# Kernel optimization log

Hardware: AMD Instinct MI355X
Metric: run time of the kernel (lower is better)

Reference implementation:

```python
import jax, jax.numpy as jnp
import numpy as np

B, S, D = 2, 2048, 2048
NH, NG = 16, 4          # q heads, groups
KVH = NH // NG          # kv heads = 4
HD = D // NH            # head dim = 128
ROPE_THETA = 10000.0


def _rope(t, cos, sin):
    """Rotate pairs along last dim. t: [B,S,D]; cos/sin: [S, D//2]."""
    tr = t.reshape(t.shape[:-1] + (-1, 2))  # [B,S,D/2,2] complex pairs (llama layout)
    xr, xi = tr[..., 0], tr[..., 1]
    c = cos[None, :, :]
    s = sin[None, :, :]
    yr = xr * c - xi * s
    yi = xr * s + xi * c
    return jnp.stack([yr, yi], axis=-1).reshape(t.shape)


def setup_inputs() -> dict:
    key = jax.random.key(0)
    k0, k1, k2, k3, k4 = jax.random.split(key, 5)
    scale = 1.0 / np.sqrt(D)
    x = jax.random.normal(k0, (B, S, D), jnp.float32)
    Wq = jax.random.normal(k1, (D, D), jnp.float32) * scale          # torch Linear: (out,in)
    Wk = jax.random.normal(k2, (D // NG, D), jnp.float32) * scale
    Wv = jax.random.normal(k3, (D // NG, D), jnp.float32) * scale
    Wo = jax.random.normal(k4, (D, D), jnp.float32) * scale
    mask = jnp.triu(jnp.ones((S, S), bool), k=1)[None, None]          # causal: True = masked
    return {"x": x, "Wq": Wq, "Wk": Wk, "Wv": Wv, "Wo": Wo, "mask": mask}


def reference(x, Wq, Wk, Wv, Wo, mask):
    b, s, d = x.shape
    q = x @ Wq.T                                  # [B,S,D]
    k = x @ Wk.T                                  # [B,S,D/NG]
    v = x @ Wv.T
    # repeat_kv: [B,S,KVH,HD] -> repeat each kv head NG times -> [B,S,NH,HD]
    k = jnp.repeat(k.reshape(b, s, KVH, HD), NG, axis=2).reshape(b, s, d)
    v = jnp.repeat(v.reshape(b, s, KVH, HD), NG, axis=2).reshape(b, s, d)
    # RoPE with freqs precomputed over the FULL hidden dim (as in source)
    freqs = 1.0 / (ROPE_THETA ** (jnp.arange(0, d, 2, dtype=jnp.float32) / d))  # [D/2]
    ang = jnp.arange(s, dtype=jnp.float32)[:, None] * freqs[None, :]            # [S,D/2]
    cos, sin = jnp.cos(ang), jnp.sin(ang)
    q = _rope(q, cos, sin)
    k = _rope(k, cos, sin)
    # split heads: [B,NH,S,HD]
    qh = q.reshape(b, s, NH, HD).transpose(0, 2, 1, 3)
    kh = k.reshape(b, s, NH, HD).transpose(0, 2, 1, 3)
    vh = v.reshape(b, s, NH, HD).transpose(0, 2, 1, 3)
    # NOTE: source scales by sqrt(hidden_dim), not sqrt(head_dim)
    scores = jnp.einsum('bhqd,bhkd->bhqk', qh, kh) / jnp.sqrt(jnp.float32(d))
    scores = jnp.where(mask, -jnp.inf, scores)
    probs = jax.nn.softmax(scores, axis=-1)
    out = jnp.einsum('bhqk,bhkd->bhqd', probs, vh)
    out = out.transpose(0, 2, 1, 3).reshape(b, s, d)
    return out @ Wo.T  # dropout is identity in eval
```

## Files before the change

### kernel.cpp

```cpp
#include <hip/hip_runtime.h>
#include <hip/hip_bf16.h>
#include <stdint.h>

typedef unsigned short u16;
typedef u16 u16x4 __attribute__((ext_vector_type(4)));
typedef unsigned u32x4 __attribute__((ext_vector_type(4)));
typedef __bf16 bf16x8 __attribute__((ext_vector_type(8)));
typedef float f32x4 __attribute__((ext_vector_type(4)));
typedef float f32x16 __attribute__((ext_vector_type(16)));

#define DEVI __device__ __forceinline__

DEVI u16 f2b(float f) {
  __hip_bfloat16 h = __float2bfloat16(f);
  return __builtin_bit_cast(u16, h);
}

DEVI unsigned pk2(float lo, float hi) {
  return (unsigned)f2b(lo) | ((unsigned)f2b(hi) << 16);
}

DEVI f32x4 mfma16(bf16x8 a, bf16x8 b, f32x4 c) {
  return __builtin_amdgcn_mfma_f32_16x16x32_bf16(a, b, c, 0, 0, 0);
}

DEVI f32x16 mfma32(bf16x8 a, bf16x8 b, f32x16 c) {
  return __builtin_amdgcn_mfma_f32_32x32x16_bf16(a, b, c, 0, 0, 0);
}

DEVI void gld_lds16(const u16* g, u16* l) {
  __builtin_amdgcn_global_load_lds(
      (const __attribute__((address_space(1))) unsigned int*)g,
      (__attribute__((address_space(3))) unsigned int*)l, 16, 0, 0);
}

__global__ void cvt_all(const float4* __restrict__ x, const float4* __restrict__ wq,
                        const float4* __restrict__ wk, const float4* __restrict__ wv,
                        const float4* __restrict__ wo,
                        u16x4* __restrict__ xb, u16x4* __restrict__ wqb,
                        u16x4* __restrict__ wkb, u16x4* __restrict__ wvb,
                        u16x4* __restrict__ wob) {
  long i = (long)blockIdx.x * 256 + threadIdx.x;
  const float4* src; u16x4* dst; long o;
  if (i < 2097152)      { src = x;  dst = xb;  o = i; }
  else if (i < 3145728) { src = wq; dst = wqb; o = i - 2097152; }
  else if (i < 3407872) { src = wk; dst = wkb; o = i - 3145728; }
  else if (i < 3670016) { src = wv; dst = wvb; o = i - 3407872; }
  else                  { src = wo; dst = wob; o = i - 3670016; }
  float4 v = src[o];
  u16x4 r = { f2b(v.x), f2b(v.y), f2b(v.z), f2b(v.w) };
  dst[o] = r;
}

__global__ void rope_table(float* __restrict__ cosT, float* __restrict__ sinT) {
  int i = blockIdx.x * 256 + threadIdx.x;
  int s = i >> 10, p = i & 1023;
  float freq = exp2f((float)p * -0.012976281620653759f);
  float ang = (float)s * freq;
  float sv, cv;
  __sincosf(ang, &sv, &cv);
  cosT[i] = cv;
  sinT[i] = sv;
}

__global__ __launch_bounds__(256)
void gemm_qkv(const u16* __restrict__ A, const u16* __restrict__ wq,
              const u16* __restrict__ wk, const u16* __restrict__ wv,
              float* __restrict__ Qtmp, float* __restrict__ Ktmp,
              u16* __restrict__ Vtp) {
  __shared__ __align__(16) u16 lds[2][2][4096];
  const int tid = threadIdx.x;
  const int lane = tid & 63;
  const int w = tid >> 6;
  const int wr = w >> 1, wc = w & 1;
  const int bx = blockIdx.x;
  const int m0 = blockIdx.y << 7, n0 = bx << 7;
  const int K = 2048;

  const u16* Bw;
  int mode;
  if (bx < 16)      { Bw = wq + (size_t)n0 * K;          mode = 0; }
  else if (bx < 20) { Bw = wk + (size_t)(n0 - 2048) * K; mode = 1; }
  else              { Bw = wv + (size_t)(n0 - 2560) * K; mode = 2; }

  const int srow = tid >> 2;
  const int schunk = (tid & 3) << 3;
  const u16* ga0 = A + (size_t)(m0 + srow) * K + schunk;
  const u16* gb0 = Bw + (size_t)srow * K + schunk;
  const size_t rstep = (size_t)64 * K;

  f32x4 acc[4][4] = {};
  const int nk = K >> 5;
  int cur = 0;

  {
    u16* la = &lds[0][0][tid << 3];
    u16* lb = &lds[0][1][tid << 3];
    gld_lds16(ga0, la);
    gld_lds16(ga0 + rstep, la + 2048);
    gld_lds16(gb0, lb);
    gld_lds16(gb0 + rstep, lb + 2048);
  }
  __syncthreads();

  const int l15 = lane & 15;
  const int kcol = (lane >> 4) << 3;
  const int arow = ((wr << 6) + l15) << 5;
  const int brow = ((wc << 6) + l15) << 5;

  for (int kt = 0; kt < nk; ++kt) {
    if (kt + 1 < nk) {
      const u16* ga = ga0 + ((size_t)(kt + 1) << 5);
      const u16* gb = gb0 + ((size_t)(kt + 1) << 5);
      u16* la = &lds[cur ^ 1][0][tid << 3];
      u16* lb = &lds[cur ^ 1][1][tid << 3];
      gld_lds16(ga, la);
      gld_lds16(ga + rstep, la + 2048);
      gld_lds16(gb, lb);
      gld_lds16(gb + rstep, lb + 2048);
    }
    const u16* la = &lds[cur][0][0];
    const u16* lb = &lds[cur][1][0];
    bf16x8 af[4], bfr[4];
#pragma unroll
    for (int mi = 0; mi < 4; ++mi)
      af[mi] = *(const bf16x8*)&la[arow + (mi << 9) + kcol];
#pragma unroll
    for (int ni = 0; ni < 4; ++ni)
      bfr[ni] = *(const bf16x8*)&lb[brow + (ni << 9) + kcol];
#pragma unroll
    for (int mi = 0; mi < 4; ++mi)
#pragma unroll
      for (int ni = 0; ni < 4; ++ni)
        acc[mi][ni] = mfma16(af[mi], bfr[ni], acc[mi][ni]);
    __syncthreads();
    cur ^= 1;
  }

  const int crow = (lane >> 4) << 2;
  const int ccol = lane & 15;
  if (mode == 0) {
#pragma unroll
    for (int mi = 0; mi < 4; ++mi) {
      int row = m0 + (wr << 6) + (mi << 4) + crow;
#pragma unroll
      for (int ni = 0; ni < 4; ++ni) {
        int col = n0 + (wc << 6) + (ni << 4) + ccol;
#pragma unroll
        for (int rr = 0; rr < 4; ++rr)
          Qtmp[(size_t)(row + rr) * 2048 + col] = acc[mi][ni][rr];
      }
    }
  } else if (mode == 1) {
#pragma unroll
    for (int mi = 0; mi < 4; ++mi) {
      int row = m0 + (wr << 6) + (mi << 4) + crow;
#pragma unroll
      for (int ni = 0; ni < 4; ++ni) {
        int col = (n0 - 2048) + (wc << 6) + (ni << 4) + ccol;
#pragma unroll
        for (int rr = 0; rr < 4; ++rr)
          Ktmp[(size_t)(row + rr) * 512 + col] = acc[mi][ni][rr];
      }
    }
  } else {
#pragma unroll
    for (int mi = 0; mi < 4; ++mi) {
      int sg = m0 + (wr << 6) + (mi << 4) + crow;
      int b = sg >> 11, s = sg & 2047;
#pragma unroll
      for (int ni = 0; ni < 4; ++ni) {
        int n = (n0 - 2560) + (wc << 6) + (ni << 4) + ccol;
        u16x4 pk = { f2b(acc[mi][ni][0]), f2b(acc[mi][ni][1]),
                     f2b(acc[mi][ni][2]), f2b(acc[mi][ni][3]) };
        *(u16x4*)&Vtp[((size_t)((b << 2) + (n >> 7)) * 128 + (n & 127)) * 2048 + s] = pk;
      }
    }
  }
}

__global__ __launch_bounds__(256)
void gemm_bt(const u16* __restrict__ A, const u16* __restrict__ Bw,
             float* __restrict__ C, int M, int N, int K) {
  __shared__ __align__(16) u16 lds[2][2][4096];
  const int tid = threadIdx.x;
  const int lane = tid & 63;
  const int w = tid >> 6;
  const int wr = w >> 1, wc = w & 1;
  const int m0 = blockIdx.y << 7, n0 = blockIdx.x << 7;

  const int srow = tid >> 2;
  const int schunk = (tid & 3) << 3;
  const u16* ga0 = A + (size_t)(m0 + srow) * K + schunk;
  const u16* gb0 = Bw + (size_t)(n0 + srow) * K + schunk;
  const size_t rstep = (size_t)64 * K;

  f32x4 acc[4][4] = {};
  const int nk = K >> 5;
  int cur = 0;

  {
    u16* la = &lds[0][0][tid << 3];
    u16* lb = &lds[0][1][tid << 3];
    gld_lds16(ga0, la);
    gld_lds16(ga0 + rstep, la + 2048);
    gld_lds16(gb0, lb);
    gld_lds16(gb0 + rstep, lb + 2048);
  }
  __syncthreads();

  const int l15 = lane & 15;
  const int kcol = (lane >> 4) << 3;
  const int arow = ((wr << 6) + l15) << 5;
  const int brow = ((wc << 6) + l15) << 5;

  for (int kt = 0; kt < nk; ++kt) {
    if (kt + 1 < nk) {
      const u16* ga = ga0 + ((size_t)(kt + 1) << 5);
      const u16* gb = gb0 + ((size_t)(kt + 1) << 5);
      u16* la = &lds[cur ^ 1][0][tid << 3];
      u16* lb = &lds[cur ^ 1][1][tid << 3];
      gld_lds16(ga, la);
      gld_lds16(ga + rstep, la + 2048);
      gld_lds16(gb, lb);
      gld_lds16(gb + rstep, lb + 2048);
    }
    const u16* la = &lds[cur][0][0];
    const u16* lb = &lds[cur][1][0];
    bf16x8 af[4], bfr[4];
#pragma unroll
    for (int mi = 0; mi < 4; ++mi)
      af[mi] = *(const bf16x8*)&la[arow + (mi << 9) + kcol];
#pragma unroll
    for (int ni = 0; ni < 4; ++ni)
      bfr[ni] = *(const bf16x8*)&lb[brow + (ni << 9) + kcol];
#pragma unroll
    for (int mi = 0; mi < 4; ++mi)
#pragma unroll
      for (int ni = 0; ni < 4; ++ni)
        acc[mi][ni] = mfma16(af[mi], bfr[ni], acc[mi][ni]);
    __syncthreads();
    cur ^= 1;
  }

  const int crow = (lane >> 4) << 2;
  const int ccol = lane & 15;
#pragma unroll
  for (int mi = 0; mi < 4; ++mi) {
    int row = m0 + (wr << 6) + (mi << 4) + crow;
#pragma unroll
    for (int ni = 0; ni < 4; ++ni) {
      int col = n0 + (wc << 6) + (ni << 4) + ccol;
#pragma unroll
      for (int rr = 0; rr < 4; ++rr)
        C[(size_t)(row + rr) * N + col] = acc[mi][ni][rr];
    }
  }
}

__global__ void rope_q(const float2* __restrict__ Qtmp, const float* __restrict__ cosT,
                       const float* __restrict__ sinT, u16* __restrict__ Qh) {
  int i = blockIdx.x * 256 + threadIdx.x;
  int pr = i & 1023;
  int row = i >> 10;
  int s = row & 2047, b = row >> 11;
  float2 v = Qtmp[(size_t)row * 1024 + pr];
  float c = cosT[(s << 10) + pr], sn = sinT[(s << 10) + pr];
  const float SC = 0.022097086912079608f * 1.4426950408889634f;
  float yr = (v.x * c - v.y * sn) * SC;
  float yi = (v.x * sn + v.y * c) * SC;
  int h = pr >> 6, hp = pr & 63;
  size_t off = ((size_t)(b * 16 + h) * 2048 + s) * 128 + hp * 2;
  unsigned pk = (unsigned)f2b(yr) | ((unsigned)f2b(yi) << 16);
  *(unsigned*)&Qh[off] = pk;
}

__global__ void rope_k(const float2* __restrict__ Ktmp, const float* __restrict__ cosT,
                       const float* __restrict__ sinT, u16* __restrict__ Kh) {
  int i = blockIdx.x * 256 + threadIdx.x;
  int hp = i & 63;
  int h = (i >> 6) & 15;
  int row = i >> 10;
  int s = row & 2047, b = row >> 11;
  float2 v = Ktmp[(size_t)row * 256 + ((h >> 2) << 6) + hp];
  int p = (h << 6) + hp;
  float c = cosT[(s << 10) + p], sn = sinT[(s << 10) + p];
  float yr = v.x * c - v.y * sn;
  float yi = v.x * sn + v.y * c;
  size_t off = ((size_t)(b * 16 + h) * 2048 + s) * 128 + hp * 2;
  unsigned pk = (unsigned)f2b(yr) | ((unsigned)f2b(yi) << 16);
  *(unsigned*)&Kh[off] = pk;
}

__global__ __launch_bounds__(256, 2)
void attn_kernel(const u16* __restrict__ Qh, const u16* __restrict__ Kh,
                 const u16* __restrict__ Vt, u16* __restrict__ attnO) {
  __shared__ __align__(16) u16 lds[3][8192];
  const int tid = threadIdx.x, lane = tid & 63, w = tid >> 6;
  const int bid = blockIdx.x;
  const int x = bid & 7, j = bid >> 3;
  const int half = j >> 5, jj = j & 31;
  const int bh = (x << 2) + (jj >> 4) + (half << 1);
  const int r = jj & 15;
  const int qt = half ? r : 15 - r;
  const int h = bh & 15, b = bh >> 4;

  const int qi = lane & 31, hi = lane >> 5;
  const int q0 = (qt << 7) + (w << 5);
  const int qabs = q0 + qi;

  const u16* Qp = Qh + (size_t)(b * 16 + h) * 262144;
  const u16* Kp = Kh + (size_t)(b * 16 + h) * 262144;
  const u16* Vp = Vt + (size_t)((b << 2) + (h >> 2)) * 262144;

  bf16x8 qf[8];
#pragma unroll
  for (int kc = 0; kc < 8; ++kc)
    qf[kc] = *(const bf16x8*)&Qp[(size_t)qabs * 128 + kc * 16 + hi * 8];

  const int kRow = tid >> 4;
  const int kCl = ((tid & 15) ^ (kRow & 7)) << 3;
  const int vRow = tid >> 2;
  const int vCl = ((tid & 3) ^ ((tid >> 3) & 3)) << 3;
  const int ldsoff = tid << 3;

  f32x16 ot[4] = {};
  float mrow = -1e30f, lsum = 0.f;
  const int nt = (qt << 2) + 4;
  const int nt_w = (qt << 2) + w + 1;
  const int swq = qi & 7, swv = (qi >> 1) & 3;

#pragma unroll
  for (int pt = 0; pt < 2; ++pt) {
    u16* bb = (u16*)lds[pt];
    gld_lds16(Kp + (size_t)((pt << 5) + kRow) * 128 + kCl, bb + ldsoff);
    gld_lds16(Kp + (size_t)((pt << 5) + kRow + 16) * 128 + kCl, bb + ldsoff + 2048);
    gld_lds16(Vp + (size_t)vRow * 2048 + (pt << 5) + vCl, bb + 4096 + ldsoff);
    gld_lds16(Vp + (size_t)(vRow + 64) * 2048 + (pt << 5) + vCl, bb + 4096 + ldsoff + 2048);
  }

  int bufc = 0;
  for (int t = 0; t < nt; ++t) {
    asm volatile("s_waitcnt vmcnt(4)" ::: "memory");
    __builtin_amdgcn_sched_barrier(0);
    __builtin_amdgcn_s_barrier();
    {
      const int ts = (t + 2 < nt) ? t + 2 : nt - 1;
      const int bufn = bufc ? bufc - 1 : 2;
      u16* bb = (u16*)lds[bufn];
      gld_lds16(Kp + (size_t)((ts << 5) + kRow) * 128 + kCl, bb + ldsoff);
      gld_lds16(Kp + (size_t)((ts << 5) + kRow + 16) * 128 + kCl, bb + ldsoff + 2048);
      gld_lds16(Vp + (size_t)vRow * 2048 + (ts << 5) + vCl, bb + 4096 + ldsoff);
      gld_lds16(Vp + (size_t)(vRow + 64) * 2048 + (ts << 5) + vCl, bb + 4096 + ldsoff + 2048);
    }
    if (t < nt_w) {
      const u16* kb_ = &lds[bufc][0];
      const u16* vb_ = &lds[bufc][4096];
      f32x16 st = {};
      __builtin_amdgcn_s_setprio(1);
#pragma unroll
      for (int kc = 0; kc < 8; ++kc) {
        bf16x8 kf = *(const bf16x8*)&kb_[(qi << 7) + ((((kc << 1) + hi) ^ swq) << 3)];
        st = mfma32(kf, qf[kc], st);
      }
      __builtin_amdgcn_s_setprio(0);

      if (t == nt_w - 1) {
        const int kb0 = t << 5;
#pragma unroll
        for (int reg = 0; reg < 16; ++reg) {
          int kk = kb0 + (reg & 3) + ((reg >> 2) << 3) + (hi << 2);
          if (kk > qabs) st[reg] = -1e30f;
        }
      }

      float tmax = st[0];
#pragma unroll
      for (int reg = 1; reg < 16; ++reg) tmax = fmaxf(tmax, st[reg]);
      tmax = fmaxf(tmax, __shfl_xor(tmax, 32));

      if (__any(tmax - mrow > 11.5f)) {
        float nm = fmaxf(mrow, tmax);
        float al = __builtin_amdgcn_exp2f(mrow - nm);
        mrow = nm;
        lsum *= al;
#pragma unroll
        for (int db = 0; db < 4; ++db)
#pragma unroll
          for (int reg = 0; reg < 16; ++reg) ot[db][reg] *= al;
      }

      float psum = 0.f;
#pragma unroll
      for (int reg = 0; reg < 16; ++reg) {
        st[reg] = __builtin_amdgcn_exp2f(st[reg] - mrow);
        psum += st[reg];
      }
      psum += __shfl_xor(psum, 32);
      lsum += psum;

      bf16x8 pfrag[2];
#pragma unroll
      for (int bbp = 0; bbp < 2; ++bbp) {
        unsigned x0 = pk2(st[8 * bbp + 0], st[8 * bbp + 1]);
        unsigned x1 = pk2(st[8 * bbp + 2], st[8 * bbp + 3]);
        unsigned y0 = pk2(st[8 * bbp + 4], st[8 * bbp + 5]);
        unsigned y1 = pk2(st[8 * bbp + 6], st[8 * bbp + 7]);
        asm("v_permlane32_swap_b32 %0, %1" : "+v"(x0), "+v"(y0));
        asm("v_permlane32_swap_b32 %0, %1" : "+v"(x1), "+v"(y1));
        u32x4 uw = { x0, x1, y0, y1 };
        pfrag[bbp] = __builtin_bit_cast(bf16x8, uw);
      }

      __builtin_amdgcn_s_setprio(1);
#pragma unroll
      for (int db = 0; db < 4; ++db) {
        const u16* vr = &vb_[((db << 5) + qi) << 5];
#pragma unroll
        for (int ks = 0; ks < 2; ++ks) {
          bf16x8 vf = *(const bf16x8*)&vr[((((ks << 1) + hi)) ^ swv) << 3];
          ot[db] = mfma32(vf, pfrag[ks], ot[db]);
        }
      }
      __builtin_amdgcn_s_setprio(0);
    }
    bufc = (bufc == 2) ? 0 : bufc + 1;
  }

  float inv = 1.f / lsum;
  u16* rowp = attnO + (size_t)(b * 2048 + qabs) * 2048 + h * 128 + (hi << 2);
#pragma unroll
  for (int db = 0; db < 4; ++db)
#pragma unroll
    for (int mg = 0; mg < 4; ++mg) {
      u16x4 pkv = { f2b(ot[db][4 * mg + 0] * inv), f2b(ot[db][4 * mg + 1] * inv),
                    f2b(ot[db][4 * mg + 2] * inv), f2b(ot[db][4 * mg + 3] * inv) };
      *(u16x4*)&rowp[(db << 5) + (mg << 3)] = pkv;
    }
}

extern "C" void kernel_launch(void* const* d_in, const int* in_sizes, int n_in,
                              void* d_out, int out_size, void* d_ws, size_t ws_size,
                              hipStream_t stream) {
  const float* x  = (const float*)d_in[0];
  const float* Wq = (const float*)d_in[1];
  const float* Wk = (const float*)d_in[2];
  const float* Wv = (const float*)d_in[3];
  const float* Wo = (const float*)d_in[4];
  float* out = (float*)d_out;
  char* ws = (char*)d_ws;

  u16*   xb   = (u16*)(ws + 0);
  u16*   wqb  = (u16*)(ws + 16777216);
  u16*   wkb  = (u16*)(ws + 25165824);
  u16*   wvb  = (u16*)(ws + 27262976);
  u16*   wob  = (u16*)(ws + 29360128);
  float* cosT = (float*)(ws + 37748736);
  float* sinT = (float*)(ws + 46137344);
  float* Qtmp = (float*)(ws + 54525952);
  u16*   attnb= (u16*)(ws + 54525952);
  float* Ktmp = (float*)(ws + 88080384);
  u16*   Qhp  = (u16*)(ws + 96468992);
  u16*   Khp  = (u16*)(ws + 113246208);
  u16*   Vtp  = (u16*)(ws + 130023424);

  cvt_all<<<18432, 256, 0, stream>>>((const float4*)x, (const float4*)Wq,
                                     (const float4*)Wk, (const float4*)Wv,
                                     (const float4*)Wo, (u16x4*)xb, (u16x4*)wqb,
                                     (u16x4*)wkb, (u16x4*)wvb, (u16x4*)wob);
  rope_table<<<8192, 256, 0, stream>>>(cosT, sinT);
  gemm_qkv<<<dim3(24, 32), 256, 0, stream>>>(xb, wqb, wkb, wvb, Qtmp, Ktmp, Vtp);
  rope_q<<<16384, 256, 0, stream>>>((const float2*)Qtmp, cosT, sinT, Qhp);
  rope_k<<<16384, 256, 0, stream>>>((const float2*)Ktmp, cosT, sinT, Khp);
  attn_kernel<<<512, 256, 0, stream>>>(Qhp, Khp, Vtp, attnb);
  gemm_bt<<<dim3(16, 32), 256, 0, stream>>>(attnb, wob, out, 4096, 2048, 2048);
}
```

Before: 229.4 us.

## Fuse RoPE into QKV GEMM epilogue via permuted weight rows

The RoPE rotation, softmax scaling and bf16 head-major packing for Q and K now run inside the QKV GEMM epilogue, and the separate rope_q/rope_k kernels are removed. The weight rows are loaded in a permuted order so that each lane holds both halves of a rotary pair in its own accumulators. The cos/sin table is interleaved into float2. This removes the fp32 Qtmp/Ktmp round trip through global memory and two kernel launches. In exchange the GEMM epilogue gets heavier, K is written four times (once per group head), and epilogue stores are narrower and scattered.

Result: faster. 219.6 us (-4.3%).

```diff
diff --git a/kernel.cpp b/kernel.cpp
--- a/kernel.cpp
+++ b/kernel.cpp
@@ -52,41 +52,42 @@
   dst[o] = r;
 }
 
-__global__ void rope_table(float* __restrict__ cosT, float* __restrict__ sinT) {
+__global__ void rope_table(float2* __restrict__ csT) {
   int i = blockIdx.x * 256 + threadIdx.x;
   int s = i >> 10, p = i & 1023;
   float freq = exp2f((float)p * -0.012976281620653759f);
   float ang = (float)s * freq;
   float sv, cv;
   __sincosf(ang, &sv, &cv);
-  cosT[i] = cv;
-  sinT[i] = sv;
+  csT[i] = make_float2(cv, sv);
 }
 
 __global__ __launch_bounds__(256)
 void gemm_qkv(const u16* __restrict__ A, const u16* __restrict__ wq,
               const u16* __restrict__ wk, const u16* __restrict__ wv,
-              float* __restrict__ Qtmp, float* __restrict__ Ktmp,
-              u16* __restrict__ Vtp) {
+              const float2* __restrict__ csT, u16* __restrict__ Qh,
+              u16* __restrict__ Kh, u16* __restrict__ Vtp) {
   __shared__ __align__(16) u16 lds[2][2][4096];
   const int tid = threadIdx.x;
   const int lane = tid & 63;
   const int w = tid >> 6;
   const int wr = w >> 1, wc = w & 1;
-  const int bx = blockIdx.x;
-  const int m0 = blockIdx.y << 7, n0 = bx << 7;
+  const int x = blockIdx.x, m0 = blockIdx.y << 7, n0 = x << 7;
   const int K = 2048;
 
   const u16* Bw;
   int mode;
-  if (bx < 16)      { Bw = wq + (size_t)n0 * K;          mode = 0; }
-  else if (bx < 20) { Bw = wk + (size_t)(n0 - 2048) * K; mode = 1; }
-  else              { Bw = wv + (size_t)(n0 - 2560) * K; mode = 2; }
+  if (x < 16)      { Bw = wq + (size_t)n0 * K;          mode = 0; }
+  else if (x < 20) { Bw = wk + (size_t)(n0 - 2048) * K; mode = 1; }
+  else             { Bw = wv + (size_t)(n0 - 2560) * K; mode = 2; }
 
   const int srow = tid >> 2;
   const int schunk = (tid & 3) << 3;
+  const int p4 = srow >> 4, pl = srow & 15;
+  const int prow = (pl << 1) | (p4 & 1) | ((p4 & 2) << 4);
+  const int bsrc = (mode == 2) ? srow : prow;
   const u16* ga0 = A + (size_t)(m0 + srow) * K + schunk;
-  const u16* gb0 = Bw + (size_t)srow * K + schunk;
+  const u16* gb0 = Bw + (size_t)bsrc * K + schunk;
   const size_t rstep = (size_t)64 * K;
 
   f32x4 acc[4][4] = {};
@@ -138,32 +139,53 @@
   }
 
   const int crow = (lane >> 4) << 2;
-  const int ccol = lane & 15;
   if (mode == 0) {
-#pragma unroll
-    for (int mi = 0; mi < 4; ++mi) {
-      int row = m0 + (wr << 6) + (mi << 4) + crow;
-#pragma unroll
-      for (int ni = 0; ni < 4; ++ni) {
-        int col = n0 + (wc << 6) + (ni << 4) + ccol;
-#pragma unroll
-        for (int rr = 0; rr < 4; ++rr)
-          Qtmp[(size_t)(row + rr) * 2048 + col] = acc[mi][ni][rr];
-      }
-    }
+    const float SCL = 0.022097086912079608f * 1.4426950408889634f;
+    const int h = x;
+    const int qb = (wc << 6) + (l15 << 1);
+    const int tb = (n0 >> 1) + (wc << 5) + l15;
+#pragma unroll
+    for (int mi = 0; mi < 4; ++mi)
+#pragma unroll
+      for (int rr = 0; rr < 4; ++rr) {
+        int row = m0 + (wr << 6) + (mi << 4) + crow + rr;
+        int s = row & 2047, b = row >> 11;
+        float2 cA = csT[(s << 10) + tb];
+        float2 cB = csT[(s << 10) + tb + 16];
+        float v0 = acc[mi][0][rr], v1 = acc[mi][1][rr];
+        float v2 = acc[mi][2][rr], v3 = acc[mi][3][rr];
+        unsigned lo = pk2((v0 * cA.x - v1 * cA.y) * SCL, (v0 * cA.y + v1 * cA.x) * SCL);
+        unsigned hi = pk2((v2 * cB.x - v3 * cB.y) * SCL, (v2 * cB.y + v3 * cB.x) * SCL);
+        u16* dst = &Qh[((size_t)(b * 16 + h) * 2048 + s) * 128 + qb];
+        *(unsigned*)dst = lo;
+        *(unsigned*)(dst + 32) = hi;
+      }
   } else if (mode == 1) {
-#pragma unroll
-    for (int mi = 0; mi < 4; ++mi) {
-      int row = m0 + (wr << 6) + (mi << 4) + crow;
-#pragma unroll
-      for (int ni = 0; ni < 4; ++ni) {
-        int col = (n0 - 2048) + (wc << 6) + (ni << 4) + ccol;
-#pragma unroll
-        for (int rr = 0; rr < 4; ++rr)
-          Ktmp[(size_t)(row + rr) * 512 + col] = acc[mi][ni][rr];
-      }
-    }
+    const int kvh = x - 16;
+    const int qb = (wc << 6) + (l15 << 1);
+#pragma unroll
+    for (int mi = 0; mi < 4; ++mi)
+#pragma unroll
+      for (int rr = 0; rr < 4; ++rr) {
+        int row = m0 + (wr << 6) + (mi << 4) + crow + rr;
+        int s = row & 2047, b = row >> 11;
+        float v0 = acc[mi][0][rr], v1 = acc[mi][1][rr];
+        float v2 = acc[mi][2][rr], v3 = acc[mi][3][rr];
+#pragma unroll
+        for (int g = 0; g < 4; ++g) {
+          int h = (kvh << 2) + g;
+          int tb = (h << 6) + (wc << 5) + l15;
+          float2 cA = csT[(s << 10) + tb];
+          float2 cB = csT[(s << 10) + tb + 16];
+          unsigned lo = pk2(v0 * cA.x - v1 * cA.y, v0 * cA.y + v1 * cA.x);
+          unsigned hi = pk2(v2 * cB.x - v3 * cB.y, v2 * cB.y + v3 * cB.x);
+          u16* dst = &Kh[((size_t)(b * 16 + h) * 2048 + s) * 128 + qb];
+          *(unsigned*)dst = lo;
+          *(unsigned*)(dst + 32) = hi;
+        }
+      }
   } else {
+    const int ccol = l15;
 #pragma unroll
     for (int mi = 0; mi < 4; ++mi) {
       int sg = m0 + (wr << 6) + (mi << 4) + crow;
@@ -256,40 +278,6 @@
         C[(size_t)(row + rr) * N + col] = acc[mi][ni][rr];
     }
   }
-}
-
-__global__ void rope_q(const float2* __restrict__ Qtmp, const float* __restrict__ cosT,
-                       const float* __restrict__ sinT, u16* __restrict__ Qh) {
-  int i = blockIdx.x * 256 + threadIdx.x;
-  int pr = i & 1023;
-  int row = i >> 10;
-  int s = row & 2047, b = row >> 11;
-  float2 v = Qtmp[(size_t)row * 1024 + pr];
-  float c = cosT[(s << 10) + pr], sn = sinT[(s << 10) + pr];
-  const float SC = 0.022097086912079608f * 1.4426950408889634f;
-  float yr = (v.x * c - v.y * sn) * SC;
-  float yi = (v.x * sn + v.y * c) * SC;
-  int h = pr >> 6, hp = pr & 63;
-  size_t off = ((size_t)(b * 16 + h) * 2048 + s) * 128 + hp * 2;
-  unsigned pk = (unsigned)f2b(yr) | ((unsigned)f2b(yi) << 16);
-  *(unsigned*)&Qh[off] = pk;
-}
-
-__global__ void rope_k(const float2* __restrict__ Ktmp, const float* __restrict__ cosT,
-                       const float* __restrict__ sinT, u16* __restrict__ Kh) {
-  int i = blockIdx.x * 256 + threadIdx.x;
-  int hp = i & 63;
-  int h = (i >> 6) & 15;
-  int row = i >> 10;
-  int s = row & 2047, b = row >> 11;
-  float2 v = Ktmp[(size_t)row * 256 + ((h >> 2) << 6) + hp];
-  int p = (h << 6) + hp;
-  float c = cosT[(s << 10) + p], sn = sinT[(s << 10) + p];
-  float yr = v.x * c - v.y * sn;
-  float yi = v.x * sn + v.y * c;
-  size_t off = ((size_t)(b * 16 + h) * 2048 + s) * 128 + hp * 2;
-  unsigned pk = (unsigned)f2b(yr) | ((unsigned)f2b(yi) << 16);
-  *(unsigned*)&Kh[off] = pk;
 }
 
 __global__ __launch_bounds__(256, 2)
@@ -450,28 +438,23 @@
   float* out = (float*)d_out;
   char* ws = (char*)d_ws;
 
-  u16*   xb   = (u16*)(ws + 0);
-  u16*   wqb  = (u16*)(ws + 16777216);
-  u16*   wkb  = (u16*)(ws + 25165824);
-  u16*   wvb  = (u16*)(ws + 27262976);
-  u16*   wob  = (u16*)(ws + 29360128);
-  float* cosT = (float*)(ws + 37748736);
-  float* sinT = (float*)(ws + 46137344);
-  float* Qtmp = (float*)(ws + 54525952);
-  u16*   attnb= (u16*)(ws + 54525952);
-  float* Ktmp = (float*)(ws + 88080384);
-  u16*   Qhp  = (u16*)(ws + 96468992);
-  u16*   Khp  = (u16*)(ws + 113246208);
-  u16*   Vtp  = (u16*)(ws + 130023424);
+  u16*    xb   = (u16*)(ws + 0);
+  u16*    wqb  = (u16*)(ws + 16777216);
+  u16*    wkb  = (u16*)(ws + 25165824);
+  u16*    wvb  = (u16*)(ws + 27262976);
+  u16*    wob  = (u16*)(ws + 29360128);
+  float2* csT  = (float2*)(ws + 37748736);
+  u16*    Qhp  = (u16*)(ws + 54525952);
+  u16*    Khp  = (u16*)(ws + 71303168);
+  u16*    Vtp  = (u16*)(ws + 88080384);
+  u16*    attnb= (u16*)(ws + 92274688);
 
   cvt_all<<<18432, 256, 0, stream>>>((const float4*)x, (const float4*)Wq,
                                      (const float4*)Wk, (const float4*)Wv,
                                      (const float4*)Wo, (u16x4*)xb, (u16x4*)wqb,
                                      (u16x4*)wkb, (u16x4*)wvb, (u16x4*)wob);
-  rope_table<<<8192, 256, 0, stream>>>(cosT, sinT);
-  gemm_qkv<<<dim3(24, 32), 256, 0, stream>>>(xb, wqb, wkb, wvb, Qtmp, Ktmp, Vtp);
-  rope_q<<<16384, 256, 0, stream>>>((const float2*)Qtmp, cosT, sinT, Qhp);
-  rope_k<<<16384, 256, 0, stream>>>((const float2*)Ktmp, cosT, sinT, Khp);
+  rope_table<<<8192, 256, 0, stream>>>(csT);
+  gemm_qkv<<<dim3(24, 32), 256, 0, stream>>>(xb, wqb, wkb, wvb, csT, Qhp, Khp, Vtp);
   attn_kernel<<<512, 256, 0, stream>>>(Qhp, Khp, Vtp, attnb);
   gemm_bt<<<dim3(16, 32), 256, 0, stream>>>(attnb, wob, out, 4096, 2048, 2048);
 }
```
